# Optimization experiments

Measured on AMD Instinct MI355X. Metric: run time of the kernel, lower is better.

The kernel has to match this reference:

```python
import jax, jax.numpy as jnp
import numpy as np

D_MODEL = 1024
N_HEADS = 16
HEAD_DIM = D_MODEL // N_HEADS
D_C = 128
THETA = 10000.0


def rope_cos_sin(timestamps):
    # timestamps: (B, L) -> cos, sin: (B, L, HEAD_DIM)
    freqs = 1.0 / (THETA ** (jnp.arange(0, HEAD_DIM, 2, dtype=jnp.float32) / HEAD_DIM))
    t = timestamps[..., None] * freqs            # (B, L, HEAD_DIM//2)
    emb = jnp.concatenate([t, t], axis=-1)       # (B, L, HEAD_DIM)
    return jnp.cos(emb), jnp.sin(emb)


def rotate_half(x):
    x1, x2 = jnp.split(x, 2, axis=-1)
    return jnp.concatenate([-x2, x1], axis=-1)


def setup_inputs() -> dict:
    key = jax.random.key(0)
    ks = jax.random.split(key, 10)
    B, L = 2, 2048
    s = 0.02
    return {
        "query": jax.random.normal(ks[0], (B, L, D_MODEL), jnp.float32),
        "timestamps_q": jax.random.uniform(ks[1], (B, L), jnp.float32) * 365.0,
        "timestamps_kv": jax.random.uniform(ks[2], (B, L), jnp.float32) * 365.0,
        "w_kv_c": jax.random.normal(ks[3], (D_MODEL, D_C), jnp.float32) * s,
        "w_kc_up": jax.random.normal(ks[4], (D_C, D_MODEL), jnp.float32) * s,
        "w_vc_up": jax.random.normal(ks[5], (D_C, D_MODEL), jnp.float32) * s,
        "w_qr": jax.random.normal(ks[6], (D_MODEL, D_MODEL), jnp.float32) * s,
        "w_kr": jax.random.normal(ks[7], (D_MODEL, D_MODEL), jnp.float32) * s,
        "w_o": jax.random.normal(ks[8], (D_MODEL, D_MODEL), jnp.float32) * s,
    }


def reference(query, timestamps_q, timestamps_kv, w_kv_c, w_kc_up, w_vc_up, w_qr, w_kr, w_o):
    B, Lq, _ = query.shape
    key_value = query  # self-attention path (key_value defaults to query)
    Lk = key_value.shape[1]

    def heads(x, L):  # (B, L, D) -> (B, H, L, hd)
        return x.reshape(B, L, N_HEADS, HEAD_DIM).transpose(0, 2, 1, 3)

    c_kv = key_value @ w_kv_c                      # (B, Lk, d_c) low-rank KV
    k_c = heads(c_kv @ w_kc_up, Lk)
    v_c = heads(c_kv @ w_vc_up, Lk)
    q_r = heads(query @ w_qr, Lq)
    k_r = heads(key_value @ w_kr, Lk)

    cos_q, _ = rope_cos_sin(timestamps_q)
    cos_k, _ = rope_cos_sin(timestamps_kv)
    cos_q = cos_q[:, None]                          # (B, 1, Lq, hd)
    cos_k = cos_k[:, None]                          # (B, 1, Lk, hd)
    # Faithful to original (which passes cos_k in the `sin` slot):
    q_r = q_r * cos_q + rotate_half(q_r) * cos_k
    k_r = k_r * cos_q + rotate_half(k_r) * cos_k

    scale = HEAD_DIM ** -0.5
    qs = q_r * scale
    attn = jnp.einsum("bhqd,bhkd->bhqk", qs, k_c) + jnp.einsum("bhqd,bhkd->bhqk", qs, k_r)
    attn_weights = jax.nn.softmax(attn, axis=-1)
    out = jnp.einsum("bhqk,bhkd->bhqd", attn_weights, v_c)
    out = out.transpose(0, 2, 1, 3).reshape(B, Lq, D_MODEL)
    return out @ w_o
```

## Files before the change

kernel.cpp:

```cpp
#include <hip/hip_runtime.h>

typedef float          f32x4    __attribute__((ext_vector_type(4)));
typedef float          float8v  __attribute__((ext_vector_type(8)));
typedef unsigned short ushort8v __attribute__((ext_vector_type(8)));
typedef __bf16         bf16x8   __attribute__((ext_vector_type(8)));

__device__ __forceinline__ unsigned short f2b(float x) {
  union { __bf16 b; unsigned short u; } v;
  v.b = (__bf16)x;
  return v.u;
}
__device__ __forceinline__ float b2f(unsigned short h) {
  union { unsigned u; float f; } v; v.u = ((unsigned)h) << 16;
  return v.f;
}

__device__ __forceinline__ void g2lds16(const unsigned short* g,
                                        unsigned short* l) {
  __builtin_amdgcn_global_load_lds(
      (const __attribute__((address_space(1))) unsigned int*)g,
      (__attribute__((address_space(3))) unsigned int*)l, 16, 0, 0);
}

__global__ void cvt_kernel(const float* __restrict__ src,
                           unsigned short* __restrict__ dst, int n8) {
  int i = blockIdx.x * 256 + threadIdx.x;
  if (i >= n8) return;
  float8v v = reinterpret_cast<const float8v*>(src)[i];
  ushort8v h;
#pragma unroll
  for (int j = 0; j < 8; ++j) h[j] = f2b(v[j]);
  reinterpret_cast<ushort8v*>(dst)[i] = h;
}

__global__ __launch_bounds__(256) void wtrans_kernel(
    const float* __restrict__ W, unsigned short* __restrict__ WT,
    int K, int N) {
  __shared__ unsigned short T[64 * 72];
  const int tid = threadIdx.x;
  const int n0 = blockIdx.x * 64, k0 = blockIdx.y * 64;
#pragma unroll
  for (int it = 0; it < 2; ++it) {
    int c = tid + it * 256;
    int r = c >> 3, cc = c & 7;
    float8v v = *reinterpret_cast<const float8v*>(
        &W[(size_t)(k0 + r) * N + n0 + cc * 8]);
    ushort8v h;
#pragma unroll
    for (int j = 0; j < 8; ++j) h[j] = f2b(v[j]);
    *reinterpret_cast<ushort8v*>(&T[r * 72 + cc * 8]) = h;
  }
  __syncthreads();
#pragma unroll
  for (int it = 0; it < 2; ++it) {
    int c = tid + it * 256;
    int n = c >> 3, kc = c & 7;
    ushort8v y;
#pragma unroll
    for (int j = 0; j < 8; ++j) y[j] = T[(kc * 8 + j) * 72 + n];
    *reinterpret_cast<ushort8v*>(&WT[(size_t)(n0 + n) * K + k0 + kc * 8]) = y;
  }
}

template <int TM, typename CT, bool ACC>
__global__ __launch_bounds__(256) void gemm_bt(
    const unsigned short* __restrict__ A, const unsigned short* __restrict__ Bt,
    CT* __restrict__ C, int M, int N, int K) {
  __shared__ unsigned short As[TM * 64];
  __shared__ unsigned short Bs[128 * 64];
  const int tid = threadIdx.x;
  const int m0 = blockIdx.y * TM, n0 = blockIdx.x * 128;
  const int wave = tid >> 6, lane = tid & 63;
  const int wm = (wave >> 1) * (TM / 2), wn = (wave & 1) * 64;
  const int l16 = lane & 15, quad = lane >> 4;
  constexpr int MI = TM / 32;

  f32x4 acc[MI][4];
#pragma unroll
  for (int i = 0; i < MI; ++i)
#pragma unroll
    for (int j = 0; j < 4; ++j)
#pragma unroll
      for (int r = 0; r < 4; ++r) acc[i][j][r] = 0.f;

  for (int k0 = 0; k0 < K; k0 += 64) {
    __syncthreads();
#pragma unroll
    for (int it = 0; it < TM * 8 / 256; ++it) {
      int c = it * 256 + tid;
      int m = c >> 3, kc = (c & 7) ^ (m & 7);
      g2lds16(&A[(size_t)(m0 + m) * K + k0 + kc * 8], &As[c * 8]);
    }
#pragma unroll
    for (int it = 0; it < 4; ++it) {
      int c = it * 256 + tid;
      int n = c >> 3, kc = (c & 7) ^ (n & 7);
      g2lds16(&Bt[(size_t)(n0 + n) * K + k0 + kc * 8], &Bs[c * 8]);
    }
    __syncthreads();

#pragma unroll
    for (int ks = 0; ks < 2; ++ks) {
      bf16x8 af[MI], bfr[4];
#pragma unroll
      for (int mi = 0; mi < MI; ++mi) {
        int m = wm + mi * 16 + l16;
        af[mi] = *reinterpret_cast<const bf16x8*>(
            &As[(m * 8 + ((ks * 4 + quad) ^ (m & 7))) * 8]);
      }
#pragma unroll
      for (int ni = 0; ni < 4; ++ni) {
        int n = wn + ni * 16 + l16;
        bfr[ni] = *reinterpret_cast<const bf16x8*>(
            &Bs[(n * 8 + ((ks * 4 + quad) ^ (n & 7))) * 8]);
      }
#pragma unroll
      for (int mi = 0; mi < MI; ++mi)
#pragma unroll
        for (int ni = 0; ni < 4; ++ni)
          acc[mi][ni] = __builtin_amdgcn_mfma_f32_16x16x32_bf16(
              af[mi], bfr[ni], acc[mi][ni], 0, 0, 0);
    }
  }

#pragma unroll
  for (int mi = 0; mi < MI; ++mi)
#pragma unroll
    for (int ni = 0; ni < 4; ++ni) {
      int row = m0 + wm + mi * 16 + quad * 4;
      int col = n0 + wn + ni * 16 + l16;
#pragma unroll
      for (int r = 0; r < 4; ++r) {
        size_t idx = (size_t)(row + r) * N + col;
        float val = acc[mi][ni][r];
        if constexpr (sizeof(CT) == 2) {
          if constexpr (ACC) val += b2f(C[idx]);
          C[idx] = f2b(val);
        } else {
          if constexpr (ACC) val += C[idx];
          C[idx] = val;
        }
      }
    }
}

__global__ __launch_bounds__(256) void gemm_fused3(
    const unsigned short* __restrict__ A, const unsigned short* __restrict__ Bt,
    unsigned short* __restrict__ Cq, unsigned short* __restrict__ Ck,
    unsigned short* __restrict__ Cc, int K) {
  __shared__ unsigned short As[1024 * 8];
  __shared__ unsigned short Bs[1024 * 8];
  const int tid = threadIdx.x;
  const int m0 = blockIdx.y * 128, n0 = blockIdx.x * 128;
  const int wave = tid >> 6, lane = tid & 63;
  const int wm = (wave >> 1) * 64, wn = (wave & 1) * 64;
  const int l16 = lane & 15, quad = lane >> 4;

  f32x4 acc[4][4];
#pragma unroll
  for (int i = 0; i < 4; ++i)
#pragma unroll
    for (int j = 0; j < 4; ++j)
#pragma unroll
      for (int r = 0; r < 4; ++r) acc[i][j][r] = 0.f;

  for (int k0 = 0; k0 < K; k0 += 64) {
    __syncthreads();
#pragma unroll
    for (int it = 0; it < 4; ++it) {
      int c = it * 256 + tid;
      int m = c >> 3, kc = (c & 7) ^ (m & 7);
      g2lds16(&A[(size_t)(m0 + m) * K + k0 + kc * 8], &As[c * 8]);
    }
#pragma unroll
    for (int it = 0; it < 4; ++it) {
      int c = it * 256 + tid;
      int n = c >> 3, kc = (c & 7) ^ (n & 7);
      g2lds16(&Bt[(size_t)(n0 + n) * K + k0 + kc * 8], &Bs[c * 8]);
    }
    __syncthreads();

#pragma unroll
    for (int ks = 0; ks < 2; ++ks) {
      bf16x8 af[4], bfr[4];
#pragma unroll
      for (int mi = 0; mi < 4; ++mi) {
        int m = wm + mi * 16 + l16;
        af[mi] = *reinterpret_cast<const bf16x8*>(
            &As[(m * 8 + ((ks * 4 + quad) ^ (m & 7))) * 8]);
      }
#pragma unroll
      for (int ni = 0; ni < 4; ++ni) {
        int n = wn + ni * 16 + l16;
        bfr[ni] = *reinterpret_cast<const bf16x8*>(
            &Bs[(n * 8 + ((ks * 4 + quad) ^ (n & 7))) * 8]);
      }
#pragma unroll
      for (int mi = 0; mi < 4; ++mi)
#pragma unroll
        for (int ni = 0; ni < 4; ++ni)
          acc[mi][ni] = __builtin_amdgcn_mfma_f32_16x16x32_bf16(
              af[mi], bfr[ni], acc[mi][ni], 0, 0, 0);
    }
  }

  unsigned short* dst;
  int w, cb;
  if (n0 < 1024)      { dst = Cq; w = 1024; cb = 0; }
  else if (n0 < 2048) { dst = Ck; w = 1024; cb = 1024; }
  else                { dst = Cc; w = 128;  cb = 2048; }
#pragma unroll
  for (int mi = 0; mi < 4; ++mi)
#pragma unroll
    for (int ni = 0; ni < 4; ++ni) {
      int row = m0 + wm + mi * 16 + quad * 4;
      int col = n0 - cb + wn + ni * 16 + l16;
#pragma unroll
      for (int r = 0; r < 4; ++r)
        dst[(size_t)(row + r) * w + col] = f2b(acc[mi][ni][r]);
    }
}

__global__ __launch_bounds__(256) void gemm_fused2(
    const unsigned short* __restrict__ A, const unsigned short* __restrict__ Bt,
    unsigned short* __restrict__ Ck, unsigned short* __restrict__ Cv, int K) {
  __shared__ unsigned short As[1024 * 8];
  __shared__ unsigned short Bs[1024 * 8];
  const int tid = threadIdx.x;
  const int m0 = blockIdx.y * 128, n0 = blockIdx.x * 128;
  const int wave = tid >> 6, lane = tid & 63;
  const int wm = (wave >> 1) * 64, wn = (wave & 1) * 64;
  const int l16 = lane & 15, quad = lane >> 4;

  f32x4 acc[4][4];
#pragma unroll
  for (int i = 0; i < 4; ++i)
#pragma unroll
    for (int j = 0; j < 4; ++j)
#pragma unroll
      for (int r = 0; r < 4; ++r) acc[i][j][r] = 0.f;

  for (int k0 = 0; k0 < K; k0 += 64) {
    __syncthreads();
#pragma unroll
    for (int it = 0; it < 4; ++it) {
      int c = it * 256 + tid;
      int m = c >> 3, kc = (c & 7) ^ (m & 7);
      g2lds16(&A[(size_t)(m0 + m) * K + k0 + kc * 8], &As[c * 8]);
    }
#pragma unroll
    for (int it = 0; it < 4; ++it) {
      int c = it * 256 + tid;
      int n = c >> 3, kc = (c & 7) ^ (n & 7);
      g2lds16(&Bt[(size_t)(n0 + n) * K + k0 + kc * 8], &Bs[c * 8]);
    }
    __syncthreads();

#pragma unroll
    for (int ks = 0; ks < 2; ++ks) {
      bf16x8 af[4], bfr[4];
#pragma unroll
      for (int mi = 0; mi < 4; ++mi) {
        int m = wm + mi * 16 + l16;
        af[mi] = *reinterpret_cast<const bf16x8*>(
            &As[(m * 8 + ((ks * 4 + quad) ^ (m & 7))) * 8]);
      }
#pragma unroll
      for (int ni = 0; ni < 4; ++ni) {
        int n = wn + ni * 16 + l16;
        bfr[ni] = *reinterpret_cast<const bf16x8*>(
            &Bs[(n * 8 + ((ks * 4 + quad) ^ (n & 7))) * 8]);
      }
#pragma unroll
      for (int mi = 0; mi < 4; ++mi)
#pragma unroll
        for (int ni = 0; ni < 4; ++ni)
          acc[mi][ni] = __builtin_amdgcn_mfma_f32_16x16x32_bf16(
              af[mi], bfr[ni], acc[mi][ni], 0, 0, 0);
    }
  }

  const bool first = (n0 < 1024);
  unsigned short* dst = first ? Ck : Cv;
  int cb = first ? 0 : 1024;
#pragma unroll
  for (int mi = 0; mi < 4; ++mi)
#pragma unroll
    for (int ni = 0; ni < 4; ++ni) {
      int row = m0 + wm + mi * 16 + quad * 4;
      int col = n0 - cb + wn + ni * 16 + l16;
#pragma unroll
      for (int r = 0; r < 4; ++r) {
        size_t idx = (size_t)(row + r) * 1024 + col;
        float val = acc[mi][ni][r];
        if (first) val += b2f(dst[idx]);
        dst[idx] = f2b(val);
      }
    }
}

__global__ void rope_kernel(unsigned short* __restrict__ qr,
                            unsigned short* __restrict__ kr,
                            const float* __restrict__ tq,
                            const float* __restrict__ tk) {
  int idx = blockIdx.x * 256 + threadIdx.x;
  int i = idx & 31;
  int mh = idx >> 5;
  int m = mh >> 4;
  float f = exp2f(-(float)i * (13.287712379549449f / 32.f));
  float cq = cosf(tq[m] * f);
  float ck = cosf(tk[m] * f);
  size_t base = (size_t)mh * 64;
  const float qscale = 0.18033688011112042f;
  float q1 = b2f(qr[base + i]), q2 = b2f(qr[base + i + 32]);
  float k1 = b2f(kr[base + i]), k2 = b2f(kr[base + i + 32]);
  qr[base + i]      = f2b((q1 * cq - q2 * ck) * qscale);
  qr[base + i + 32] = f2b((q2 * cq + q1 * ck) * qscale);
  kr[base + i]      = f2b(k1 * cq - k2 * ck);
  kr[base + i + 32] = f2b(k2 * cq + k1 * ck);
}

__global__ __launch_bounds__(256) void vtrans_kernel(
    const unsigned short* __restrict__ v, unsigned short* __restrict__ vt,
    int L) {
  __shared__ unsigned short T[64 * 72];
  const int tid = threadIdx.x;
  const int l0 = blockIdx.x * 64, bh = blockIdx.y;
  const size_t inbase = ((size_t)(bh >> 4) * L) * 1024 + (bh & 15) * 64;
  const size_t outbase = (size_t)bh * 64 * L;
#pragma unroll
  for (int it = 0; it < 2; ++it) {
    int c = tid + it * 256;
    int l = c >> 3, dc = c & 7;
    ushort8v x = *reinterpret_cast<const ushort8v*>(
        &v[inbase + (size_t)(l0 + l) * 1024 + dc * 8]);
    *reinterpret_cast<ushort8v*>(&T[l * 72 + dc * 8]) = x;
  }
  __syncthreads();
#pragma unroll
  for (int it = 0; it < 2; ++it) {
    int c = tid + it * 256;
    int d = c >> 3, g = c & 7;
    ushort8v y;
#pragma unroll
    for (int e = 0; e < 8; ++e) {
      int k = ((g >> 2) << 5) | ((e >> 2) << 4) | (((g >> 1) & 1) << 3) |
              ((g & 1) << 2) | (e & 3);
      y[e] = T[k * 72 + d];
    }
    *reinterpret_cast<ushort8v*>(&vt[outbase + (size_t)d * L + l0 + g * 8]) = y;
  }
}

__global__ __launch_bounds__(512) void flash15_kernel(
    const unsigned short* __restrict__ qs, const unsigned short* __restrict__ ks,
    const unsigned short* __restrict__ vt, unsigned short* __restrict__ o,
    int L) {
  __shared__ unsigned short KV[2][2][2][512 * 8];
  const int tid = threadIdx.x;
  const int wave = tid >> 6, lane = tid & 63;
  const int half = wave >> 2;
  const int l16 = lane & 15, quad = lane >> 4;
  const int bh = blockIdx.y;
  const int qb = blockIdx.x * 128 + (wave & 3) * 32;
  const size_t base = ((size_t)(bh >> 4) * L) * 1024 + (bh & 15) * 64;
  const size_t vtbase = (size_t)bh * 64 * L;
  const int kvoff = half * (L >> 1);
  const int sid = tid & 255;

  bf16x8 aq[2][2];
#pragma unroll
  for (int mt = 0; mt < 2; ++mt) {
    size_t qrow = base + (size_t)(qb + mt * 16 + l16) * 1024;
    aq[mt][0] = *reinterpret_cast<const bf16x8*>(&qs[qrow + quad * 8]);
    aq[mt][1] = *reinterpret_cast<const bf16x8*>(&qs[qrow + 32 + quad * 8]);
  }

  ushort8v onesu;
#pragma unroll
  for (int j = 0; j < 8; ++j) onesu[j] = 0x3F80;
  bf16x8 ones = *reinterpret_cast<bf16x8*>(&onesu);

  f32x4 oacc[2][4];
  f32x4 lacc[2];
#pragma unroll
  for (int mt = 0; mt < 2; ++mt) {
#pragma unroll
    for (int r = 0; r < 4; ++r) lacc[mt][r] = 0.f;
#pragma unroll
    for (int nt = 0; nt < 4; ++nt)
#pragma unroll
      for (int r = 0; r < 4; ++r) oacc[mt][nt][r] = 0.f;
  }

  const int T = L / 128;
#pragma unroll
  for (int it = 0; it < 2; ++it) {
    int c = it * 256 + sid;
    int key = c >> 3, dc = (c & 7) ^ (key & 7);
    g2lds16(&ks[base + (size_t)(kvoff + key) * 1024 + dc * 8],
            &KV[0][half][0][c * 8]);
  }
#pragma unroll
  for (int it = 0; it < 2; ++it) {
    int c = it * 256 + sid;
    int d = c >> 3, kc = (c & 7) ^ (d & 7);
    g2lds16(&vt[vtbase + (size_t)d * L + kvoff + kc * 8],
            &KV[1][half][0][c * 8]);
  }

  for (int t = 0; t < T; ++t) {
    __syncthreads();
    if (t + 1 < T) {
      int k0 = kvoff + (t + 1) * 64, nb = (t + 1) & 1;
#pragma unroll
      for (int it = 0; it < 2; ++it) {
        int c = it * 256 + sid;
        int key = c >> 3, dc = (c & 7) ^ (key & 7);
        g2lds16(&ks[base + (size_t)(k0 + key) * 1024 + dc * 8],
                &KV[0][half][nb][c * 8]);
      }
#pragma unroll
      for (int it = 0; it < 2; ++it) {
        int c = it * 256 + sid;
        int d = c >> 3, kc = (c & 7) ^ (d & 7);
        g2lds16(&vt[vtbase + (size_t)d * L + k0 + kc * 8],
                &KV[1][half][nb][c * 8]);
      }
    }
    const int cb = t & 1;
    const unsigned short* Ks = &KV[0][half][cb][0];
    const unsigned short* Vs = &KV[1][half][cb][0];

    f32x4 st[2][4];
#pragma unroll
    for (int nt = 0; nt < 4; ++nt) {
      int key = nt * 16 + l16;
      int dc0 = quad ^ (key & 7);
      int dc1 = (4 + quad) ^ (key & 7);
      bf16x8 bk0 = *reinterpret_cast<const bf16x8*>(&Ks[(key * 8 + dc0) * 8]);
      bf16x8 bk1 = *reinterpret_cast<const bf16x8*>(&Ks[(key * 8 + dc1) * 8]);
#pragma unroll
      for (int mt = 0; mt < 2; ++mt) {
        f32x4 z; z[0] = z[1] = z[2] = z[3] = 0.f;
        z = __builtin_amdgcn_mfma_f32_16x16x32_bf16(bk0, aq[mt][0], z, 0, 0, 0);
        z = __builtin_amdgcn_mfma_f32_16x16x32_bf16(bk1, aq[mt][1], z, 0, 0, 0);
        st[mt][nt] = z;
      }
    }

    bf16x8 ap[2][2];
#pragma unroll
    for (int mt = 0; mt < 2; ++mt) {
#pragma unroll
      for (int hf = 0; hf < 2; ++hf)
#pragma unroll
        for (int w = 0; w < 4; ++w) {
          int nt = 2 * hf + (w >> 1), p = w & 1;
          ap[mt][hf][2 * w] =
              (__bf16)__builtin_amdgcn_exp2f(st[mt][nt][2 * p]);
          ap[mt][hf][2 * w + 1] =
              (__bf16)__builtin_amdgcn_exp2f(st[mt][nt][2 * p + 1]);
        }
      lacc[mt] = __builtin_amdgcn_mfma_f32_16x16x32_bf16(ap[mt][0], ones,
                                                         lacc[mt], 0, 0, 0);
      lacc[mt] = __builtin_amdgcn_mfma_f32_16x16x32_bf16(ap[mt][1], ones,
                                                         lacc[mt], 0, 0, 0);
    }

#pragma unroll
    for (int nt = 0; nt < 4; ++nt) {
      int d = nt * 16 + l16;
#pragma unroll
      for (int hf = 0; hf < 2; ++hf) {
        int kc = (hf * 4 + quad) ^ (d & 7);
        bf16x8 bv = *reinterpret_cast<const bf16x8*>(&Vs[(d * 8 + kc) * 8]);
#pragma unroll
        for (int mt = 0; mt < 2; ++mt)
          oacc[mt][nt] = __builtin_amdgcn_mfma_f32_16x16x32_bf16(
              ap[mt][hf], bv, oacc[mt][nt], 0, 0, 0);
      }
    }
  }

  __syncthreads();
  float* cbuf = (float*)&KV[0][0][0][0];
  if (half == 1) {
    int slot = ((wave - 4) * 64 + lane) * 44;
#pragma unroll
    for (int mt = 0; mt < 2; ++mt) {
#pragma unroll
      for (int nt = 0; nt < 4; ++nt)
        *reinterpret_cast<f32x4*>(&cbuf[slot + (mt * 4 + nt) * 4]) =
            oacc[mt][nt];
      *reinterpret_cast<f32x4*>(&cbuf[slot + 32 + mt * 4]) = lacc[mt];
    }
  }
  __syncthreads();
  if (half == 0) {
    int slot = (wave * 64 + lane) * 44;
#pragma unroll
    for (int mt = 0; mt < 2; ++mt) {
#pragma unroll
      for (int nt = 0; nt < 4; ++nt) {
        f32x4 ov = *reinterpret_cast<const f32x4*>(
            &cbuf[slot + (mt * 4 + nt) * 4]);
#pragma unroll
        for (int r = 0; r < 4; ++r) oacc[mt][nt][r] += ov[r];
      }
      f32x4 lv = *reinterpret_cast<const f32x4*>(&cbuf[slot + 32 + mt * 4]);
#pragma unroll
      for (int r = 0; r < 4; ++r) lacc[mt][r] += lv[r];
    }
#pragma unroll
    for (int mt = 0; mt < 2; ++mt)
#pragma unroll
      for (int r = 0; r < 4; ++r) {
        float inv = __builtin_amdgcn_rcpf(lacc[mt][r]);
        int q = qb + mt * 16 + quad * 4 + r;
#pragma unroll
        for (int nt = 0; nt < 4; ++nt)
          o[base + (size_t)q * 1024 + nt * 16 + l16] =
              f2b(oacc[mt][nt][r] * inv);
      }
  }
}

extern "C" void kernel_launch(void* const* d_in, const int* in_sizes, int n_in,
                              void* d_out, int out_size, void* d_ws, size_t ws_size,
                              hipStream_t stream) {
  const float* X    = (const float*)d_in[0];
  const float* tq   = (const float*)d_in[1];
  const float* tk   = (const float*)d_in[2];
  const float* wkvc = (const float*)d_in[3];
  const float* wkc  = (const float*)d_in[4];
  const float* wvc  = (const float*)d_in[5];
  const float* wqr  = (const float*)d_in[6];
  const float* wkr  = (const float*)d_in[7];
  const float* wo   = (const float*)d_in[8];

  const int D = 1024, DC = 128, L = 2048;
  const int M = in_sizes[0] / D;
  const int B = M / L;
  const int NBH = B * 16;
  (void)n_in; (void)out_size; (void)ws_size;

  unsigned short* p = (unsigned short*)d_ws;
  auto take = [&](size_t n) { unsigned short* r = p; p += n; return r; };
  unsigned short* Xb    = take((size_t)M * D);
  unsigned short* qsb   = take((size_t)M * D);
  unsigned short* ksb   = take((size_t)M * D);
  unsigned short* vcb   = take((size_t)M * D);
  unsigned short* ckv   = take((size_t)M * DC);
  unsigned short* Wbig  = take((size_t)(2 * D + DC) * D);
  unsigned short* Wkcvc = take((size_t)(2 * D) * DC);
  unsigned short* WoT   = take((size_t)D * D);
  unsigned short* vtb   = Xb;
  unsigned short* obuf  = vcb;

  cvt_kernel<<<(M * D / 8 + 255) / 256, 256, 0, stream>>>(X, Xb, M * D / 8);
  auto wt = [&](const float* W, unsigned short* WT, int K, int N) {
    dim3 g(N / 64, K / 64);
    wtrans_kernel<<<g, 256, 0, stream>>>(W, WT, K, N);
  };
  wt(wqr,  Wbig,                          D, D);
  wt(wkr,  Wbig + (size_t)D * D,          D, D);
  wt(wkvc, Wbig + (size_t)2 * D * D,      D, DC);
  wt(wkc,  Wkcvc,                         DC, D);
  wt(wvc,  Wkcvc + (size_t)D * DC,        DC, D);
  wt(wo,   WoT,                           D, D);

  {
    dim3 g((2 * D + DC) / 128, M / 128);
    gemm_fused3<<<g, 256, 0, stream>>>(Xb, Wbig, qsb, ksb, ckv, D);
  }
  rope_kernel<<<(M * 512) / 256, 256, 0, stream>>>(qsb, ksb, tq, tk);
  {
    dim3 g(2 * D / 128, M / 128);
    gemm_fused2<<<g, 256, 0, stream>>>(ckv, Wkcvc, ksb, vcb, DC);
  }

  dim3 tg(L / 64, NBH);
  vtrans_kernel<<<tg, 256, 0, stream>>>(vcb, vtb, L);

  dim3 fg(L / 128, NBH);
  flash15_kernel<<<fg, 512, 0, stream>>>(qsb, ksb, vtb, obuf, L);

  {
    dim3 g(D / 128, M / 64);
    gemm_bt<64, float, false><<<g, 256, 0, stream>>>(
        obuf, WoT, (float*)d_out, M, D, D);
  }
}
```

Measured before the change: 222.0 us.

## Merge prep conversions into one launch and fuse RoPE into projection GEMM epilogue

Replaces the activation conversion and six weight-transpose launches with a single prep kernel that dispatches on block index. Moves the RoPE rotation and query scaling into the epilogue of the fused QKV projection GEMM, which works because each wave's 64-column tile covers a full head so the paired halves sit in the same registers. This drops six kernel launches and a separate read-modify-write pass over the q and k buffers. The cost is more cos evaluations and scattered timestamp loads in the GEMM epilogue, plus a more branchy prep kernel.

```diff
diff --git a/kernel.cpp b/kernel.cpp
--- a/kernel.cpp
+++ b/kernel.cpp
@@ -22,23 +22,37 @@
       (__attribute__((address_space(3))) unsigned int*)l, 16, 0, 0);
 }
 
-__global__ void cvt_kernel(const float* __restrict__ src,
-                           unsigned short* __restrict__ dst, int n8) {
-  int i = blockIdx.x * 256 + threadIdx.x;
-  if (i >= n8) return;
-  float8v v = reinterpret_cast<const float8v*>(src)[i];
-  ushort8v h;
-#pragma unroll
-  for (int j = 0; j < 8; ++j) h[j] = f2b(v[j]);
-  reinterpret_cast<ushort8v*>(dst)[i] = h;
-}
-
-__global__ __launch_bounds__(256) void wtrans_kernel(
-    const float* __restrict__ W, unsigned short* __restrict__ WT,
-    int K, int N) {
+__global__ __launch_bounds__(256) void prep_kernel(
+    const float* __restrict__ X, unsigned short* __restrict__ Xb, int cvtb,
+    int n8,
+    const float* __restrict__ w0, unsigned short* __restrict__ t0,
+    const float* __restrict__ w1, unsigned short* __restrict__ t1,
+    const float* __restrict__ w2, unsigned short* __restrict__ t2,
+    const float* __restrict__ w3, unsigned short* __restrict__ t3,
+    const float* __restrict__ w4, unsigned short* __restrict__ t4,
+    const float* __restrict__ w5, unsigned short* __restrict__ t5) {
   __shared__ unsigned short T[64 * 72];
   const int tid = threadIdx.x;
-  const int n0 = blockIdx.x * 64, k0 = blockIdx.y * 64;
+  int blk = blockIdx.x;
+  if (blk < cvtb) {
+    int i = blk * 256 + tid;
+    if (i >= n8) return;
+    float8v v = reinterpret_cast<const float8v*>(X)[i];
+    ushort8v h;
+#pragma unroll
+    for (int j = 0; j < 8; ++j) h[j] = f2b(v[j]);
+    reinterpret_cast<ushort8v*>(Xb)[i] = h;
+    return;
+  }
+  blk -= cvtb;
+  const float* W; unsigned short* WT; int K, N, bx, by;
+  if (blk < 256)      { W = w0; WT = t0; K = 1024; N = 1024; bx = blk & 15;         by = blk >> 4; }
+  else if (blk < 512) { W = w1; WT = t1; K = 1024; N = 1024; bx = (blk - 256) & 15; by = (blk - 256) >> 4; }
+  else if (blk < 544) { W = w2; WT = t2; K = 1024; N = 128;  bx = (blk - 512) & 1;  by = (blk - 512) >> 1; }
+  else if (blk < 576) { W = w3; WT = t3; K = 128;  N = 1024; bx = (blk - 544) & 15; by = (blk - 544) >> 4; }
+  else if (blk < 608) { W = w4; WT = t4; K = 128;  N = 1024; bx = (blk - 576) & 15; by = (blk - 576) >> 4; }
+  else                { W = w5; WT = t5; K = 1024; N = 1024; bx = (blk - 608) & 15; by = (blk - 608) >> 4; }
+  const int n0 = bx * 64, k0 = by * 64;
 #pragma unroll
   for (int it = 0; it < 2; ++it) {
     int c = tid + it * 256;
@@ -147,7 +161,8 @@
 __global__ __launch_bounds__(256) void gemm_fused3(
     const unsigned short* __restrict__ A, const unsigned short* __restrict__ Bt,
     unsigned short* __restrict__ Cq, unsigned short* __restrict__ Ck,
-    unsigned short* __restrict__ Cc, int K) {
+    unsigned short* __restrict__ Cc, const float* __restrict__ tq,
+    const float* __restrict__ tk, int K) {
   __shared__ unsigned short As[1024 * 8];
   __shared__ unsigned short Bs[1024 * 8];
   const int tid = threadIdx.x;
@@ -204,21 +219,41 @@
     }
   }
 
-  unsigned short* dst;
-  int w, cb;
-  if (n0 < 1024)      { dst = Cq; w = 1024; cb = 0; }
-  else if (n0 < 2048) { dst = Ck; w = 1024; cb = 1024; }
-  else                { dst = Cc; w = 128;  cb = 2048; }
-#pragma unroll
-  for (int mi = 0; mi < 4; ++mi)
-#pragma unroll
-    for (int ni = 0; ni < 4; ++ni) {
-      int row = m0 + wm + mi * 16 + quad * 4;
-      int col = n0 - cb + wn + ni * 16 + l16;
-#pragma unroll
-      for (int r = 0; r < 4; ++r)
-        dst[(size_t)(row + r) * w + col] = f2b(acc[mi][ni][r]);
-    }
+  if (n0 < 2048) {
+    const bool isq = (n0 < 1024);
+    unsigned short* dst = isq ? Cq : Ck;
+    const int cb = isq ? 0 : 1024;
+    const float s = isq ? 0.18033688011112042f : 1.0f;
+    const float f0 = exp2f(-(float)l16 * (13.287712379549449f / 32.f));
+    const float f1 = exp2f(-(float)(l16 + 16) * (13.287712379549449f / 32.f));
+#pragma unroll
+    for (int mi = 0; mi < 4; ++mi)
+#pragma unroll
+      for (int r = 0; r < 4; ++r) {
+        int row = m0 + wm + mi * 16 + quad * 4 + r;
+        float tqm = tq[row], tkm = tk[row];
+#pragma unroll
+        for (int np = 0; np < 2; ++np) {
+          float f = np ? f1 : f0;
+          float cq = cosf(tqm * f), ck = cosf(tkm * f);
+          float v1 = acc[mi][np][r], v2 = acc[mi][np + 2][r];
+          int col = n0 - cb + wn + np * 16 + l16;
+          dst[(size_t)row * 1024 + col]      = f2b((v1 * cq - v2 * ck) * s);
+          dst[(size_t)row * 1024 + col + 32] = f2b((v2 * cq + v1 * ck) * s);
+        }
+      }
+  } else {
+#pragma unroll
+    for (int mi = 0; mi < 4; ++mi)
+#pragma unroll
+      for (int ni = 0; ni < 4; ++ni) {
+        int row = m0 + wm + mi * 16 + quad * 4;
+        int col = n0 - 2048 + wn + ni * 16 + l16;
+#pragma unroll
+        for (int r = 0; r < 4; ++r)
+          Cc[(size_t)(row + r) * 128 + col] = f2b(acc[mi][ni][r]);
+      }
+  }
 }
 
 __global__ __launch_bounds__(256) void gemm_fused2(
@@ -297,27 +332,6 @@
         dst[idx] = f2b(val);
       }
     }
-}
-
-__global__ void rope_kernel(unsigned short* __restrict__ qr,
-                            unsigned short* __restrict__ kr,
-                            const float* __restrict__ tq,
-                            const float* __restrict__ tk) {
-  int idx = blockIdx.x * 256 + threadIdx.x;
-  int i = idx & 31;
-  int mh = idx >> 5;
-  int m = mh >> 4;
-  float f = exp2f(-(float)i * (13.287712379549449f / 32.f));
-  float cq = cosf(tq[m] * f);
-  float ck = cosf(tk[m] * f);
-  size_t base = (size_t)mh * 64;
-  const float qscale = 0.18033688011112042f;
-  float q1 = b2f(qr[base + i]), q2 = b2f(qr[base + i + 32]);
-  float k1 = b2f(kr[base + i]), k2 = b2f(kr[base + i + 32]);
-  qr[base + i]      = f2b((q1 * cq - q2 * ck) * qscale);
-  qr[base + i + 32] = f2b((q2 * cq + q1 * ck) * qscale);
-  kr[base + i]      = f2b(k1 * cq - k2 * ck);
-  kr[base + i + 32] = f2b(k2 * cq + k1 * ck);
 }
 
 __global__ __launch_bounds__(256) void vtrans_kernel(
@@ -558,23 +572,21 @@
   unsigned short* vtb   = Xb;
   unsigned short* obuf  = vcb;
 
-  cvt_kernel<<<(M * D / 8 + 255) / 256, 256, 0, stream>>>(X, Xb, M * D / 8);
-  auto wt = [&](const float* W, unsigned short* WT, int K, int N) {
-    dim3 g(N / 64, K / 64);
-    wtrans_kernel<<<g, 256, 0, stream>>>(W, WT, K, N);
-  };
-  wt(wqr,  Wbig,                          D, D);
-  wt(wkr,  Wbig + (size_t)D * D,          D, D);
-  wt(wkvc, Wbig + (size_t)2 * D * D,      D, DC);
-  wt(wkc,  Wkcvc,                         DC, D);
-  wt(wvc,  Wkcvc + (size_t)D * DC,        DC, D);
-  wt(wo,   WoT,                           D, D);
+  const int n8 = M * D / 8;
+  const int cvtb = (n8 + 255) / 256;
+  prep_kernel<<<cvtb + 864, 256, 0, stream>>>(
+      X, Xb, cvtb, n8,
+      wqr,  Wbig,
+      wkr,  Wbig + (size_t)D * D,
+      wkvc, Wbig + (size_t)2 * D * D,
+      wkc,  Wkcvc,
+      wvc,  Wkcvc + (size_t)D * DC,
+      wo,   WoT);
 
   {
     dim3 g((2 * D + DC) / 128, M / 128);
-    gemm_fused3<<<g, 256, 0, stream>>>(Xb, Wbig, qsb, ksb, ckv, D);
-  }
-  rope_kernel<<<(M * 512) / 256, 256, 0, stream>>>(qsb, ksb, tq, tk);
+    gemm_fused3<<<g, 256, 0, stream>>>(Xb, Wbig, qsb, ksb, ckv, tq, tk, D);
+  }
   {
     dim3 g(2 * D / 128, M / 128);
     gemm_fused2<<<g, 256, 0, stream>>>(ckv, Wkcvc, ksb, vcb, DC);
```

Result: slower. 322.7 us (+45.4%).
